# Optimization experiments

Measured on AMD Instinct MI355X. Metric: run time of the kernel, lower is better.

The kernel has to match this reference:

```python
import jax, jax.numpy as jnp
import numpy as np
from jax import lax

DIM = 96
D_STATE = 16
D_CONV = 4
EXPAND = 2
D_INNER = EXPAND * DIM           # 192
DT_RANK = (DIM + 15) // 16       # 6
EPS = 1e-5


def _upsample2x_align_corners(x):
    # bilinear, align_corners=True, scale_factor=2 (matches nn.Upsample)
    B, C, H, W = x.shape
    def lin_idx(n_in, n_out):
        pos = jnp.arange(n_out) * ((n_in - 1) / (n_out - 1))
        i0 = jnp.floor(pos).astype(jnp.int32)
        i1 = jnp.minimum(i0 + 1, n_in - 1)
        w = (pos - i0).astype(x.dtype)
        return i0, i1, w
    r0, r1, rw = lin_idx(H, 2 * H)
    c0, c1, cw = lin_idx(W, 2 * W)
    xr = x[:, :, r0, :] * (1 - rw)[None, None, :, None] + x[:, :, r1, :] * rw[None, None, :, None]
    return xr[:, :, :, c0] * (1 - cw) + xr[:, :, :, c1] * cw


def _conv2d(x, w, b, pad):
    y = lax.conv_general_dilated(x, w, (1, 1), [(pad, pad), (pad, pad)],
                                 dimension_numbers=('NCHW', 'OIHW', 'NCHW'))
    return y + b[None, :, None, None]


def _instance_norm(x):
    m = x.mean(axis=(2, 3), keepdims=True)
    v = x.var(axis=(2, 3), keepdims=True)
    return (x - m) * lax.rsqrt(v + EPS)


def _selective_scan(u, dt, A, Bm, Cm, D):
    # u, dt: [B,L,Din]; Bm, Cm: [B,L,N]; A: [Din,N]; D: [Din]
    def step(h, inp):
        u_t, dt_t, B_t, C_t = inp                       # [B,Din],[B,Din],[B,N],[B,N]
        dA = jnp.exp(dt_t[..., None] * A)               # [B,Din,N]
        h = h * dA + (dt_t * u_t)[..., None] * B_t[:, None, :]
        y = jnp.einsum('bdn,bn->bd', h, C_t)
        return h, y
    Bsz, L, Din = u.shape
    h0 = jnp.zeros((Bsz, Din, A.shape[1]), u.dtype)
    xs = (u.swapaxes(0, 1), dt.swapaxes(0, 1), Bm.swapaxes(0, 1), Cm.swapaxes(0, 1))
    _, ys = lax.scan(step, h0, xs)                      # ys: [L,B,Din]
    return ys.swapaxes(0, 1) + u * D


def _mamba(xseq, in_proj_w, conv1d_w, conv1d_b, x_proj_w, dt_proj_w, dt_proj_b,
           A_log, D, out_proj_w):
    # xseq: [B,L,dim]
    xz = xseq @ in_proj_w.T                             # [B,L,2*Din]
    xin, z = jnp.split(xz, 2, axis=-1)
    xc = xin.swapaxes(1, 2)                             # [B,Din,L]
    xc = lax.conv_general_dilated(xc, conv1d_w, (1,), [(D_CONV - 1, 0)],
                                  dimension_numbers=('NCH', 'OIH', 'NCH'),
                                  feature_group_count=D_INNER)
    xc = xc + conv1d_b[None, :, None]
    u = jax.nn.silu(xc.swapaxes(1, 2))                  # [B,L,Din]
    x_dbl = u @ x_proj_w.T                              # [B,L,dt_rank+2N]
    dt, Bm, Cm = jnp.split(x_dbl, [DT_RANK, DT_RANK + D_STATE], axis=-1)
    dt = jax.nn.softplus(dt @ dt_proj_w.T + dt_proj_b)  # [B,L,Din]
    A = -jnp.exp(A_log)                                 # [Din,N]
    y = _selective_scan(u, dt, A, Bm, Cm, D)
    y = y * jax.nn.silu(z)
    return y @ out_proj_w.T                             # [B,L,dim]


def setup_inputs() -> dict:
    key = jax.random.key(0)
    ks = jax.random.split(key, 16)
    s = 0.05
    inp = {
        'x': jax.random.normal(ks[0], (2, DIM, 64, 64), jnp.float32),
        'Hx': jax.random.normal(ks[1], (2, DIM * 2, 128, 128), jnp.float32),
        'conv1_w': jax.random.normal(ks[2], (DIM, DIM * 3, 1, 1), jnp.float32) * s,
        'conv1_b': jax.random.normal(ks[3], (DIM,), jnp.float32) * s,
        'conv2_w': jax.random.normal(ks[4], (DIM, DIM, 3, 3), jnp.float32) * s,
        'conv2_b': jax.random.normal(ks[5], (DIM,), jnp.float32) * s,
        'conv3_w': jax.random.normal(ks[6], (DIM, DIM, 1, 1), jnp.float32) * s,
        'conv3_b': jax.random.normal(ks[7], (DIM,), jnp.float32) * s,
        'in_proj_w': jax.random.normal(ks[8], (2 * D_INNER, DIM), jnp.float32) * s,
        'conv1d_w': jax.random.normal(ks[9], (D_INNER, 1, D_CONV), jnp.float32) * s,
        'conv1d_b': jax.random.normal(ks[10], (D_INNER,), jnp.float32) * s,
        'x_proj_w': jax.random.normal(ks[11], (DT_RANK + 2 * D_STATE, D_INNER), jnp.float32) * s,
        'dt_proj_w': jax.random.normal(ks[12], (D_INNER, DT_RANK), jnp.float32) * s,
        'dt_proj_b': jax.random.normal(ks[13], (D_INNER,), jnp.float32) * 0.1,
        'A_log': jnp.log(jnp.tile(jnp.arange(1, D_STATE + 1, dtype=jnp.float32)[None, :], (D_INNER, 1))),
        'D': jnp.ones((D_INNER,), jnp.float32),
        'out_proj_w': jax.random.normal(ks[14], (DIM, D_INNER), jnp.float32) * s,
    }
    return inp


def reference(x, Hx, conv1_w, conv1_b, conv2_w, conv2_b, conv3_w, conv3_b,
              in_proj_w, conv1d_w, conv1d_b, x_proj_w, dt_proj_w, dt_proj_b,
              A_log, D, out_proj_w):
    up = _upsample2x_align_corners(x)                   # [B,dim,H,W]
    cat = jnp.concatenate([up, Hx], axis=1)             # [B,3*dim,H,W]
    h = _conv2d(cat, conv1_w, conv1_b, 0)
    h = _conv2d(h, conv2_w, conv2_b, 1)
    h = _conv2d(h, conv3_w, conv3_b, 0)
    Lx = jax.nn.selu(_instance_norm(h))                 # [B,dim,H,W]
    B, C, H, W = Lx.shape
    seq = Lx.reshape(B, C, H * W).swapaxes(1, 2)        # [B,L,dim]
    y = _mamba(seq, in_proj_w, conv1d_w, conv1d_b, x_proj_w, dt_proj_w,
               dt_proj_b, A_log, D, out_proj_w)
    return y.swapaxes(1, 2).reshape(B, C, H, W) + Lx
```

## Files before the change

### kernel.cpp

```cpp
#include <hip/hip_runtime.h>
#include <hip/hip_bf16.h>
#include <math.h>

#define LSEQ 16384
#define DIN  192
#define GCH  512
#define TCH  32

typedef float f4v __attribute__((ext_vector_type(4)));
typedef short s8v __attribute__((ext_vector_type(8)));
typedef unsigned short u16x8 __attribute__((ext_vector_type(8)));

__device__ __forceinline__ float siluf(float x) { return __fdividef(x, 1.0f + __expf(-x)); }
__device__ __forceinline__ float fexp2(float x) {
#if __has_builtin(__builtin_amdgcn_exp2f)
  return __builtin_amdgcn_exp2f(x);
#else
  return __expf(x * 0.69314718056f);
#endif
}
__device__ __forceinline__ unsigned short f2bf(float f) {
  unsigned int u = __float_as_uint(f);
  unsigned int r = (u + 0x7FFFu + ((u >> 16) & 1u)) >> 16;
  return (unsigned short)r;
}
__device__ __forceinline__ float bf2f(unsigned short s) {
  return __uint_as_float(((unsigned int)s) << 16);
}

__global__ __launch_bounds__(256) void k_packw(const float* __restrict__ c1w,
    const float* __restrict__ c2w, const float* __restrict__ c3w,
    const float* __restrict__ Win, const float* __restrict__ Wx,
    const float* __restrict__ Wout, unsigned short* __restrict__ P) {
  int i = blockIdx.x * 256 + threadIdx.x;
  if (i >= 184320) return;
  if (i < 27648) { P[i] = f2bf(c1w[i]); return; }
  int j = i - 27648;
  if (j < 82944) {
    int cc = j / 27648, r = j - cc * 27648;
    int kk = r / 3072, r2 = r - kk * 3072;
    int oc = r2 >> 5, icl = r2 & 31;
    int ky = kk / 3, kx = kk - ky * 3;
    P[i] = f2bf(c2w[((oc * 96 + cc * 32 + icl) * 3 + ky) * 3 + kx]);
    return;
  }
  j -= 82944;
  if (j < 9216) { P[i] = f2bf(c3w[j]); return; }
  j -= 9216;
  if (j < 36864) { P[i] = f2bf(Win[j]); return; }
  j -= 36864;
  if (j < 9216) {
    int oc = j / 192, k = j - oc * 192;
    P[i] = (oc < 38) ? f2bf(Wx[oc * 192 + k]) : (unsigned short)0;
    return;
  }
  j -= 9216;
  P[i] = f2bf(Wout[j]);
}

__global__ __launch_bounds__(256) void k_upcat(const float* __restrict__ x,
    const float* __restrict__ Hx, unsigned short* __restrict__ UH) {
  __shared__ float tile[96 * 65];
  int px0 = blockIdx.x * 64, b = blockIdx.y;
  int tid = threadIdx.x;
  for (int cg = 0; cg < 3; cg++) {
    if (cg == 0) {
      int oh = px0 >> 7, owbase = px0 & 127;
      float pr = oh * (63.0f / 127.0f);
      int r0 = (int)pr; float rw = pr - (float)r0; int r1 = min(r0 + 1, 63);
      for (int t = tid; t < 1536; t += 256) {
        int c = t >> 4, p4 = t & 15;
        const float* rp0 = x + ((size_t)b * 96 + c) * 4096 + r0 * 64;
        const float* rp1 = x + ((size_t)b * 96 + c) * 4096 + r1 * 64;
#pragma unroll
        for (int g = 0; g < 4; g++) {
          int ow = owbase + p4 * 4 + g;
          float pc = ow * (63.0f / 127.0f);
          int c0 = (int)pc; float cw = pc - (float)c0; int c1 = min(c0 + 1, 63);
          float v00 = rp0[c0], v01 = rp0[c1], v10 = rp1[c0], v11 = rp1[c1];
          float top = v00 + (v10 - v00) * rw;
          float bot = v01 + (v11 - v01) * rw;
          tile[c * 65 + p4 * 4 + g] = top + (bot - top) * cw;
        }
      }
    } else {
      for (int t = tid; t < 1536; t += 256) {
        int c = t >> 4, p4 = t & 15;
        float4 v = *(const float4*)&Hx[((size_t)b * 192 + (cg - 1) * 96 + c) * LSEQ + px0 + p4 * 4];
        tile[c * 65 + p4 * 4 + 0] = v.x;
        tile[c * 65 + p4 * 4 + 1] = v.y;
        tile[c * 65 + p4 * 4 + 2] = v.z;
        tile[c * 65 + p4 * 4 + 3] = v.w;
      }
    }
    __syncthreads();
    for (int t = tid; t < 768; t += 256) {
      int px = t / 12, c8 = t - px * 12;
      u16x8 o;
#pragma unroll
      for (int jj = 0; jj < 8; jj++) o[jj] = f2bf(tile[(c8 * 8 + jj) * 65 + px]);
      *(u16x8*)&UH[((size_t)b * LSEQ + px0 + px) * 288 + cg * 96 + c8 * 8] = o;
    }
    __syncthreads();
  }
}

#define OUT_BF16R    0
#define OUT_F32P     1
#define OUT_F32R     2
#define OUT_F32P_RES 4
#define OUT_XZ       5

template<int OM, int NT>
__global__ __launch_bounds__(256) void k_gemm(
    const unsigned short* __restrict__ X,
    const unsigned short* __restrict__ Wp, const float* __restrict__ bias,
    void* __restrict__ outv, void* __restrict__ outv2, const float* __restrict__ resid,
    int K, int ostride, int ng) {
  __shared__ unsigned short x_t[128 * 96];
  __shared__ unsigned short w_t[NT * 16 * 96];
  Wp += (size_t)blockIdx.y * 96 * K;
  int pxg0 = blockIdx.x * 128;
  int b = pxg0 >> 14, px_in0 = pxg0 & 16383;
  int tid = threadIdx.x, lane = tid & 63, wv = tid >> 6;
  int r = lane & 15, q = lane >> 4;
  f4v acc[2][NT];
#pragma unroll
  for (int mi = 0; mi < 2; mi++)
#pragma unroll
    for (int n = 0; n < NT; n++) acc[mi][n] = (f4v)0.0f;
  int nchunk = K / 96;
  for (int kc = 0; kc < nchunk; kc++) {
    for (int t = tid; t < NT * 16 * 12; t += 256) {
      int row = t / 12, u8 = t - row * 12;
      *(u16x8*)&w_t[row * 96 + u8 * 8] = *(const u16x8*)&Wp[(size_t)row * K + kc * 96 + u8 * 8];
    }
    for (int t = tid; t < 1536; t += 256) {
      int rr = t / 12, u8 = t - rr * 12;
      *(u16x8*)&x_t[rr * 96 + u8 * 8] =
          *(const u16x8*)&X[(size_t)(pxg0 + rr) * K + kc * 96 + u8 * 8];
    }
    __syncthreads();
#pragma unroll
    for (int k0 = 0; k0 < 96; k0 += 32) {
      s8v a0 = *(const s8v*)&x_t[((wv * 2 + 0) * 16 + r) * 96 + k0 + q * 8];
      s8v a1 = *(const s8v*)&x_t[((wv * 2 + 1) * 16 + r) * 96 + k0 + q * 8];
#pragma unroll
      for (int n = 0; n < NT; n++) {
        s8v bb = *(const s8v*)&w_t[(n * 16 + r) * 96 + k0 + q * 8];
        acc[0][n] = __builtin_amdgcn_mfma_f32_16x16x32_bf16(a0, bb, acc[0][n], 0, 0, 0);
        acc[1][n] = __builtin_amdgcn_mfma_f32_16x16x32_bf16(a1, bb, acc[1][n], 0, 0, 0);
      }
    }
    __syncthreads();
  }
#pragma unroll
  for (int mi = 0; mi < 2; mi++) {
    int pxl = (wv * 2 + mi) * 16 + q * 4;
    int pxg = pxg0 + pxl;
#pragma unroll
    for (int n = 0; n < NT; n++) {
      int oc = n * 16 + r;
      if (OM == OUT_BF16R) {
        float bv = bias[oc];
        unsigned short* O = (unsigned short*)outv;
#pragma unroll
        for (int g = 0; g < 4; g++)
          O[(size_t)(pxg + g) * 96 + oc] = f2bf(acc[mi][n][g] + bv);
      } else if (OM == OUT_F32P) {
        float bv = bias[oc];
        float* O = (float*)outv;
        float4 o = make_float4(acc[mi][n][0] + bv, acc[mi][n][1] + bv,
                               acc[mi][n][2] + bv, acc[mi][n][3] + bv);
        *(float4*)&O[((size_t)b * 96 + oc) * LSEQ + px_in0 + pxl] = o;
      } else if (OM == OUT_F32P_RES) {
        float* O = (float*)outv;
        size_t ad = ((size_t)b * 96 + oc) * LSEQ + px_in0 + pxl;
        float4 rv = *(const float4*)&resid[ad];
        float4 o = make_float4(acc[mi][n][0] + rv.x, acc[mi][n][1] + rv.y,
                               acc[mi][n][2] + rv.z, acc[mi][n][3] + rv.w);
        *(float4*)&O[ad] = o;
      } else if (OM == OUT_F32R) {
        float* O = (float*)outv;
        int ocg = blockIdx.y * 96 + oc;
        if (ocg < ng) {
#pragma unroll
          for (int g = 0; g < 4; g++)
            O[(size_t)(pxg + g) * ostride + ocg] = acc[mi][n][g];
        }
      } else {
        int ocg = (blockIdx.y & 1) * 96 + oc;
        if (blockIdx.y < 2) {
          float* O = (float*)outv;
#pragma unroll
          for (int g = 0; g < 4; g++)
            O[(size_t)(pxg + g) * 192 + ocg] = acc[mi][n][g];
        } else {
          unsigned short* O = (unsigned short*)outv2;
#pragma unroll
          for (int g = 0; g < 4; g++)
            O[(size_t)(pxg + g) * 192 + ocg] = f2bf(acc[mi][n][g]);
        }
      }
    }
  }
}

__global__ __launch_bounds__(256) void k_conv3x3m(const unsigned short* __restrict__ X,
    const unsigned short* __restrict__ Wp2, const float* __restrict__ bias,
    unsigned short* __restrict__ out) {
  __shared__ unsigned short in_t[3 * 68 * 32];
  __shared__ unsigned short w_t[9 * 96 * 32];
  int bi = blockIdx.x;
  int hx = bi & 1, y = (bi >> 1) & 127, b = bi >> 8;
  int px0 = hx * 64;
  int tid = threadIdx.x, lane = tid & 63, wv = tid >> 6;
  int r = lane & 15, q = lane >> 4;
  f4v acc[6];
#pragma unroll
  for (int n = 0; n < 6; n++) acc[n] = (f4v)0.0f;
  for (int cc = 0; cc < 3; cc++) {
    for (int t = tid; t < 3456; t += 256)
      *(u16x8*)&w_t[t * 8] = *(const u16x8*)&Wp2[cc * 27648 + t * 8];
    for (int t = tid; t < 792; t += 256) {
      int row = t / 264, rem = t - row * 264;
      int c_l = rem >> 2, icq = rem & 3;
      int gy = y - 1 + row, gx = px0 - 1 + c_l;
      u16x8 v = {0, 0, 0, 0, 0, 0, 0, 0};
      if (gy >= 0 && gy < 128 && gx >= 0 && gx < 128)
        v = *(const u16x8*)&X[(((size_t)b * 128 + gy) * 128 + gx) * 96 + cc * 32 + icq * 8];
      *(u16x8*)&in_t[(row * 68 + c_l) * 32 + icq * 8] = v;
    }
    __syncthreads();
#pragma unroll
    for (int kk = 0; kk < 9; kk++) {
      int ky = kk / 3, kx = kk - ky * 3;
      s8v a = *(const s8v*)&in_t[(ky * 68 + wv * 16 + r + kx) * 32 + q * 8];
#pragma unroll
      for (int n = 0; n < 6; n++) {
        s8v bb = *(const s8v*)&w_t[(kk * 96 + n * 16 + r) * 32 + q * 8];
        acc[n] = __builtin_amdgcn_mfma_f32_16x16x32_bf16(a, bb, acc[n], 0, 0, 0);
      }
    }
    __syncthreads();
  }
  size_t rowbase = ((size_t)b * 128 + y) * 128 + px0 + wv * 16 + q * 4;
#pragma unroll
  for (int n = 0; n < 6; n++) {
    int oc = n * 16 + r;
    float bv = bias[oc];
#pragma unroll
    for (int g = 0; g < 4; g++)
      out[(rowbase + g) * 96 + oc] = f2bf(acc[n][g] + bv);
  }
}

__global__ __launch_bounds__(256) void k_stats(const float* __restrict__ h, float* __restrict__ stats) {
  int bc = blockIdx.x;
  const float* p = h + (size_t)bc * LSEQ;
  float s = 0.f, ss = 0.f;
  for (int i = threadIdx.x; i < LSEQ; i += 256) { float v = p[i]; s += v; ss = fmaf(v, v, ss); }
  __shared__ float rs[256], rss[256];
  int tid = threadIdx.x;
  rs[tid] = s; rss[tid] = ss; __syncthreads();
  for (int o = 128; o > 0; o >>= 1) {
    if (tid < o) { rs[tid] += rs[tid + o]; rss[tid] += rss[tid + o]; }
    __syncthreads();
  }
  if (tid == 0) {
    float m = rs[0] * (1.0f / LSEQ);
    float var = rss[0] * (1.0f / LSEQ) - m * m;
    stats[bc * 2] = m;
    stats[bc * 2 + 1] = rsqrtf(fmaxf(var, 0.f) + 1e-5f);
  }
}

__device__ __forceinline__ float seluf(float v) {
  const float kS = 1.0507009873554805f, kSA = 1.0507009873554805f * 1.6732632423543772f;
  return v > 0.f ? kS * v : kSA * (__expf(v) - 1.f);
}
__global__ __launch_bounds__(256) void k_normselu2(const float* __restrict__ h,
    const float* __restrict__ stats, float* __restrict__ Lx, unsigned short* __restrict__ LxR) {
  __shared__ float tile[96 * 65];
  int px0 = blockIdx.x * 64, b = blockIdx.y;
  int tid = threadIdx.x;
  for (int t = tid; t < 1536; t += 256) {
    int c = t >> 4, p4 = t & 15;
    size_t ga = ((size_t)b * 96 + c) * LSEQ + px0 + p4 * 4;
    float4 v = *(const float4*)&h[ga];
    float m = stats[(b * 96 + c) * 2], rv = stats[(b * 96 + c) * 2 + 1];
    v.x = seluf((v.x - m) * rv);
    v.y = seluf((v.y - m) * rv);
    v.z = seluf((v.z - m) * rv);
    v.w = seluf((v.w - m) * rv);
    *(float4*)&Lx[ga] = v;
    tile[c * 65 + p4 * 4 + 0] = v.x;
    tile[c * 65 + p4 * 4 + 1] = v.y;
    tile[c * 65 + p4 * 4 + 2] = v.z;
    tile[c * 65 + p4 * 4 + 3] = v.w;
  }
  __syncthreads();
  for (int t = tid; t < 768; t += 256) {
    int px = t / 12, c8 = t - px * 12;
    u16x8 o;
#pragma unroll
    for (int jj = 0; jj < 8; jj++) o[jj] = f2bf(tile[(c8 * 8 + jj) * 65 + px]);
    *(u16x8*)&LxR[((size_t)b * LSEQ + px0 + px) * 96 + c8 * 8] = o;
  }
}

__global__ __launch_bounds__(256) void k_conv1d(const float* __restrict__ xzx,
    const float* __restrict__ w1d, const float* __restrict__ b1d,
    unsigned short* __restrict__ uR) {
  int gid = blockIdx.x * 256 + threadIdx.x;
  if (gid >= 2 * LSEQ * DIN) return;
  int d = gid % DIN, bl = gid / DIN;
  int l = bl & (LSEQ - 1);
  float4 w = *(const float4*)&w1d[d * 4];
  float wv[4] = {w.x, w.y, w.z, w.w};
  float acc = b1d[d];
#pragma unroll
  for (int k = 0; k < 4; k++) {
    int lk = l - 3 + k;
    if (lk >= 0) acc = fmaf(wv[k], xzx[(size_t)(bl - 3 + k) * DIN + d], acc);
  }
  uR[gid] = f2bf(siluf(acc));
}

__global__ __launch_bounds__(192, 3) void k_scanA(const unsigned short* __restrict__ uR,
    const float* __restrict__ xdbl, const float* __restrict__ Wdt,
    const float* __restrict__ bdt, const float* __restrict__ Alog,
    float* __restrict__ chA, float* __restrict__ chB) {
  int b = blockIdx.y, g = blockIdx.x, d = threadIdx.x;
  __shared__ float Bs[TCH * 16], Dts[TCH * 8];
  for (int i = d; i < TCH * 16; i += 192) {
    int t = i >> 4, n = i & 15;
    Bs[i] = xdbl[(size_t)(b * LSEQ + g * TCH + t) * 38 + 6 + n];
  }
  for (int i = d; i < TCH * 6; i += 192) {
    int t = i / 6, c = i - t * 6;
    Dts[t * 8 + c] = xdbl[(size_t)(b * LSEQ + g * TCH + t) * 38 + c];
  }
  float ac2[16];
#pragma unroll
  for (int n = 0; n < 16; n++) ac2[n] = -__expf(Alog[d * 16 + n]) * 1.44269504f;
  float wdt[6];
#pragma unroll
  for (int c = 0; c < 6; c++) wdt[c] = Wdt[d * 6 + c];
  float bd = bdt[d];
  size_t base0 = (size_t)(b * LSEQ + g * TCH);
  float uu[TCH];
#pragma unroll
  for (int t = 0; t < TCH; t++) uu[t] = bf2f(uR[(base0 + t) * DIN + d]);
  __syncthreads();
  float dtv[TCH];
#pragma unroll
  for (int t = 0; t < TCH; t++) {
    float dr = bd;
#pragma unroll
    for (int c = 0; c < 6; c++) dr = fmaf(Dts[t * 8 + c], wdt[c], dr);
    dtv[t] = dr > 20.f ? dr : __logf(1.f + __expf(dr));
  }
  float ap[16], hb[16];
#pragma unroll
  for (int n = 0; n < 16; n++) { ap[n] = 1.f; hb[n] = 0.f; }
#pragma unroll
  for (int t = 0; t < TCH; t++) {
    float du = dtv[t] * uu[t];
    float bs[16];
    const float4* src = (const float4*)&Bs[t * 16];
#pragma unroll
    for (int qq = 0; qq < 4; qq++) {
      float4 v = src[qq];
      bs[qq * 4] = v.x; bs[qq * 4 + 1] = v.y; bs[qq * 4 + 2] = v.z; bs[qq * 4 + 3] = v.w;
    }
#pragma unroll
    for (int n = 0; n < 16; n++) {
      float e = fexp2(dtv[t] * ac2[n]);
      ap[n] *= e;
      hb[n] = fmaf(hb[n], e, du * bs[n]);
    }
  }
  size_t co = ((size_t)(b * GCH + g) * DIN + d) * 16;
#pragma unroll
  for (int qq = 0; qq < 4; qq++) {
    ((float4*)(chA + co))[qq] = make_float4(ap[qq * 4], ap[qq * 4 + 1], ap[qq * 4 + 2], ap[qq * 4 + 3]);
    ((float4*)(chB + co))[qq] = make_float4(hb[qq * 4], hb[qq * 4 + 1], hb[qq * 4 + 2], hb[qq * 4 + 3]);
  }
}

__global__ __launch_bounds__(256) void k_scanB(const float* __restrict__ chA,
    const float* __restrict__ chB, float* __restrict__ h0) {
  __shared__ float sa[16 * 17], sb[16 * 17];
  int blk = blockIdx.x;
  int b = blk / DIN, d = blk - b * DIN;
  int tid = threadIdx.x;
  int seg = tid >> 4, n = tid & 15;
  float ca[32], cb[32];
  float aagg = 1.f, bagg = 0.f;
#pragma unroll 8
  for (int j = 0; j < 32; j++) {
    int g = seg * 32 + j;
    size_t off = ((size_t)(b * GCH + g) * DIN + d) * 16 + n;
    float a = chA[off], bb = chB[off];
    ca[j] = a; cb[j] = bb;
    bagg = fmaf(a, bagg, bb);
    aagg *= a;
  }
  sa[n * 17 + seg] = aagg;
  sb[n * 17 + seg] = bagg;
  __syncthreads();
  if (tid < 16) {
    float pa = 1.f, pb = 0.f;
#pragma unroll
    for (int s = 0; s < 16; s++) {
      float ta = sa[tid * 17 + s], tb = sb[tid * 17 + s];
      sa[tid * 17 + s] = pa;
      sb[tid * 17 + s] = pb;
      pb = fmaf(ta, pb, tb);
      pa *= ta;
    }
  }
  __syncthreads();
  float h = sb[n * 17 + seg];
#pragma unroll 8
  for (int j = 0; j < 32; j++) {
    int g = seg * 32 + j;
    size_t off = ((size_t)(b * GCH + g) * DIN + d) * 16 + n;
    h0[off] = h;
    h = fmaf(ca[j], h, cb[j]);
  }
}

__global__ __launch_bounds__(192, 3) void k_scanC(const unsigned short* __restrict__ uR,
    const float* __restrict__ xdbl, const float* __restrict__ Wdt,
    const float* __restrict__ bdt, const unsigned short* __restrict__ zR,
    const float* __restrict__ Alog, const float* __restrict__ Dp,
    const float* __restrict__ h0, unsigned short* __restrict__ yR) {
  int b = blockIdx.y, g = blockIdx.x, d = threadIdx.x;
  __shared__ float Bs[TCH * 16], Cs[TCH * 16], Dts[TCH * 8];
  for (int i = d; i < TCH * 16; i += 192) {
    int t = i >> 4, n = i & 15;
    size_t rb = (size_t)(b * LSEQ + g * TCH + t) * 38;
    Bs[i] = xdbl[rb + 6 + n];
    Cs[i] = xdbl[rb + 22 + n];
  }
  for (int i = d; i < TCH * 6; i += 192) {
    int t = i / 6, c = i - t * 6;
    Dts[t * 8 + c] = xdbl[(size_t)(b * LSEQ + g * TCH + t) * 38 + c];
  }
  float ac2[16];
#pragma unroll
  for (int n = 0; n < 16; n++) ac2[n] = -__expf(Alog[d * 16 + n]) * 1.44269504f;
  float wdt[6];
#pragma unroll
  for (int c = 0; c < 6; c++) wdt[c] = Wdt[d * 6 + c];
  float bd = bdt[d];
  float Dd = Dp[d];
  size_t base0 = (size_t)(b * LSEQ + g * TCH);
  float uu[TCH];
#pragma unroll
  for (int t = 0; t < TCH; t++) uu[t] = bf2f(uR[(base0 + t) * DIN + d]);
  size_t co = ((size_t)(b * GCH + g) * DIN + d) * 16;
  float h[16];
#pragma unroll
  for (int qq = 0; qq < 4; qq++) {
    float4 v = ((const float4*)(h0 + co))[qq];
    h[qq * 4] = v.x; h[qq * 4 + 1] = v.y; h[qq * 4 + 2] = v.z; h[qq * 4 + 3] = v.w;
  }
  __syncthreads();
  float dtv[TCH];
#pragma unroll
  for (int t = 0; t < TCH; t++) {
    float dr = bd;
#pragma unroll
    for (int c = 0; c < 6; c++) dr = fmaf(Dts[t * 8 + c], wdt[c], dr);
    dtv[t] = dr > 20.f ? dr : __logf(1.f + __expf(dr));
  }
#pragma unroll
  for (int t = 0; t < TCH; t++) {
    float du = dtv[t] * uu[t];
    float zv = bf2f(zR[(base0 + t) * DIN + d]);
    float bs[16], cs[16];
    const float4* sbp = (const float4*)&Bs[t * 16];
    const float4* scp = (const float4*)&Cs[t * 16];
#pragma unroll
    for (int qq = 0; qq < 4; qq++) {
      float4 vb = sbp[qq], vc = scp[qq];
      bs[qq * 4] = vb.x; bs[qq * 4 + 1] = vb.y; bs[qq * 4 + 2] = vb.z; bs[qq * 4 + 3] = vb.w;
      cs[qq * 4] = vc.x; cs[qq * 4 + 1] = vc.y; cs[qq * 4 + 2] = vc.z; cs[qq * 4 + 3] = vc.w;
    }
    float y0 = 0.f, y1 = 0.f, y2 = 0.f, y3 = 0.f;
#pragma unroll
    for (int n = 0; n < 16; n++) {
      float e = fexp2(dtv[t] * ac2[n]);
      h[n] = fmaf(h[n], e, du * bs[n]);
      float p = h[n] * cs[n];
      if ((n & 3) == 0) y0 += p; else if ((n & 3) == 1) y1 += p;
      else if ((n & 3) == 2) y2 += p; else y3 += p;
    }
    float yv = ((y0 + y1) + (y2 + y3)) + uu[t] * Dd;
    yR[(base0 + t) * DIN + d] = f2bf(yv * siluf(zv));
  }
}

extern "C" void kernel_launch(void* const* d_in, const int* in_sizes, int n_in,
                              void* d_out, int out_size, void* d_ws, size_t ws_size,
                              hipStream_t stream) {
  (void)in_sizes; (void)n_in; (void)out_size; (void)ws_size;
  const float* x    = (const float*)d_in[0];
  const float* Hx   = (const float*)d_in[1];
  const float* c1w  = (const float*)d_in[2];
  const float* c1b  = (const float*)d_in[3];
  const float* c2w  = (const float*)d_in[4];
  const float* c2b  = (const float*)d_in[5];
  const float* c3w  = (const float*)d_in[6];
  const float* c3b  = (const float*)d_in[7];
  const float* Win  = (const float*)d_in[8];
  const float* w1d  = (const float*)d_in[9];
  const float* b1d  = (const float*)d_in[10];
  const float* Wx   = (const float*)d_in[11];
  const float* Wdt  = (const float*)d_in[12];
  const float* bdt  = (const float*)d_in[13];
  const float* Alog = (const float*)d_in[14];
  const float* Dp   = (const float*)d_in[15];
  const float* Wout = (const float*)d_in[16];
  float* out = (float*)d_out;

  float* ws = (float*)d_ws;
  const size_t F = (size_t)2 * 96 * LSEQ;
  const size_t Fh = F / 2;

  float*          b_h3 = ws;
  float*          chA  = ws;
  float*          b_Lx = ws + F;
  unsigned short* R1   = (unsigned short*)(ws + 2 * F);
  unsigned short* R2   = (unsigned short*)(ws + 2 * F + Fh);
  float*          xdbl = ws + 2 * F + Fh;
  unsigned short* UH   = (unsigned short*)(ws + 3 * F);
  float*          xzx  = ws + 3 * F;
  float*          chB  = ws + 3 * F;
  unsigned short* yRb  = (unsigned short*)(ws + 3 * F);
  float*          h0b  = ws + 4 * F;
  unsigned short* zRb  = (unsigned short*)(ws + 5 * F);
  unsigned short* R3   = (unsigned short*)(ws + 6 * F);
  unsigned short* Wp   = (unsigned short*)(ws + 7 * F);
  float*          b_st = ws + 7 * F + 92160;

  k_packw<<<dim3(720), dim3(256), 0, stream>>>(c1w, c2w, c3w, Win, Wx, Wout, Wp);
  k_upcat<<<dim3(256, 2), dim3(256), 0, stream>>>(x, Hx, UH);
  k_gemm<OUT_BF16R, 6><<<dim3(256, 1), dim3(256), 0, stream>>>(
      UH, Wp, c1b, R1, nullptr, nullptr, 288, 0, 0);
  k_conv3x3m<<<dim3(512), dim3(256), 0, stream>>>(R1, Wp + 27648, c2b, R2);
  k_gemm<OUT_F32P, 6><<<dim3(256, 1), dim3(256), 0, stream>>>(
      R2, Wp + 110592, c3b, b_h3, nullptr, nullptr, 96, 0, 0);
  k_stats<<<dim3(192), dim3(256), 0, stream>>>(b_h3, b_st);
  k_normselu2<<<dim3(256, 2), dim3(256), 0, stream>>>(b_h3, b_st, b_Lx, R1);
  k_gemm<OUT_XZ, 6><<<dim3(256, 4), dim3(256), 0, stream>>>(
      R1, Wp + 119808, nullptr, xzx, zRb, nullptr, 96, 192, 0);
  k_conv1d<<<dim3((2 * LSEQ * DIN + 255) / 256), dim3(256), 0, stream>>>(xzx, w1d, b1d, R3);
  k_gemm<OUT_F32R, 3><<<dim3(256, 1), dim3(256), 0, stream>>>(
      R3, Wp + 156672, nullptr, xdbl, nullptr, nullptr, 192, 38, 38);
  k_scanA<<<dim3(GCH, 2), dim3(192), 0, stream>>>(R3, xdbl, Wdt, bdt, Alog, chA, chB);
  k_scanB<<<dim3(2 * DIN), dim3(256), 0, stream>>>(chA, chB, h0b);
  k_scanC<<<dim3(GCH, 2), dim3(192), 0, stream>>>(R3, xdbl, Wdt, bdt, zRb, Alog, Dp, h0b, yRb);
  k_gemm<OUT_F32P_RES, 6><<<dim3(256, 1), dim3(256), 0, stream>>>(
      yRb, Wp + 165888, nullptr, out, nullptr, b_Lx, 192, 0, 0);
}
```

Before: 333.9 us.

## Fuse instance-norm stats into conv3 GEMM and store xz projection as bf16

The conv3 GEMM epilogue now accumulates per-channel sum and sum-of-squares through shared-memory and global atomics, which removes the separate stats kernel. The stats buffer is zeroed inside the weight-pack kernel, and the norm kernel derives mean and rstd from the raw sums. The in_proj GEMM now uses 12 N-tiles over 2 y-blocks and writes the x branch as bf16 instead of fp32, which halves that traffic into conv1d. The scan also preloads the z values up front, and the workspace layout is reshuffled. The one-pass E[x²]−m² variance computed with float atomics may lose precision and is not deterministic.

```diff
diff --git a/kernel.cpp b/kernel.cpp
--- a/kernel.cpp
+++ b/kernel.cpp
@@ -31,9 +31,10 @@
 __global__ __launch_bounds__(256) void k_packw(const float* __restrict__ c1w,
     const float* __restrict__ c2w, const float* __restrict__ c3w,
     const float* __restrict__ Win, const float* __restrict__ Wx,
-    const float* __restrict__ Wout, unsigned short* __restrict__ P) {
+    const float* __restrict__ Wout, unsigned short* __restrict__ P,
+    float* __restrict__ st) {
   int i = blockIdx.x * 256 + threadIdx.x;
-  if (i >= 184320) return;
+  if (i >= 184320) { if (i < 184704) st[i - 184320] = 0.f; return; }
   if (i < 27648) { P[i] = f2bf(c1w[i]); return; }
   int j = i - 27648;
   if (j < 82944) {
@@ -105,11 +106,11 @@
   }
 }
 
-#define OUT_BF16R    0
-#define OUT_F32P     1
-#define OUT_F32R     2
-#define OUT_F32P_RES 4
-#define OUT_XZ       5
+#define OUT_BF16R       0
+#define OUT_F32R        2
+#define OUT_F32P_RES    4
+#define OUT_F32P_STATS  6
+#define OUT_XZB         7
 
 template<int OM, int NT>
 __global__ __launch_bounds__(256) void k_gemm(
@@ -119,7 +120,8 @@
     int K, int ostride, int ng) {
   __shared__ unsigned short x_t[128 * 96];
   __shared__ unsigned short w_t[NT * 16 * 96];
-  Wp += (size_t)blockIdx.y * 96 * K;
+  __shared__ float sstat[(OM == OUT_F32P_STATS) ? 192 : 2];
+  Wp += (size_t)blockIdx.y * NT * 16 * K;
   int pxg0 = blockIdx.x * 128;
   int b = pxg0 >> 14, px_in0 = pxg0 & 16383;
   int tid = threadIdx.x, lane = tid & 63, wv = tid >> 6;
@@ -154,6 +156,10 @@
     }
     __syncthreads();
   }
+  if (OM == OUT_F32P_STATS) {
+    if (tid < 192) sstat[tid] = 0.f;
+    __syncthreads();
+  }
 #pragma unroll
   for (int mi = 0; mi < 2; mi++) {
     int pxl = (wv * 2 + mi) * 16 + q * 4;
@@ -167,12 +173,16 @@
 #pragma unroll
         for (int g = 0; g < 4; g++)
           O[(size_t)(pxg + g) * 96 + oc] = f2bf(acc[mi][n][g] + bv);
-      } else if (OM == OUT_F32P) {
+      } else if (OM == OUT_F32P_STATS) {
         float bv = bias[oc];
         float* O = (float*)outv;
         float4 o = make_float4(acc[mi][n][0] + bv, acc[mi][n][1] + bv,
                                acc[mi][n][2] + bv, acc[mi][n][3] + bv);
         *(float4*)&O[((size_t)b * 96 + oc) * LSEQ + px_in0 + pxl] = o;
+        float s = o.x + o.y + o.z + o.w;
+        float qsum = o.x * o.x + o.y * o.y + o.z * o.z + o.w * o.w;
+        atomicAdd(&sstat[oc * 2], s);
+        atomicAdd(&sstat[oc * 2 + 1], qsum);
       } else if (OM == OUT_F32P_RES) {
         float* O = (float*)outv;
         size_t ad = ((size_t)b * 96 + oc) * LSEQ + px_in0 + pxl;
@@ -182,26 +192,26 @@
         *(float4*)&O[ad] = o;
       } else if (OM == OUT_F32R) {
         float* O = (float*)outv;
-        int ocg = blockIdx.y * 96 + oc;
+        int ocg = blockIdx.y * NT * 16 + oc;
         if (ocg < ng) {
 #pragma unroll
           for (int g = 0; g < 4; g++)
             O[(size_t)(pxg + g) * ostride + ocg] = acc[mi][n][g];
         }
       } else {
-        int ocg = (blockIdx.y & 1) * 96 + oc;
-        if (blockIdx.y < 2) {
-          float* O = (float*)outv;
-#pragma unroll
-          for (int g = 0; g < 4; g++)
-            O[(size_t)(pxg + g) * 192 + ocg] = acc[mi][n][g];
-        } else {
-          unsigned short* O = (unsigned short*)outv2;
-#pragma unroll
-          for (int g = 0; g < 4; g++)
-            O[(size_t)(pxg + g) * 192 + ocg] = f2bf(acc[mi][n][g]);
-        }
+        unsigned short* O = (blockIdx.y == 0) ? (unsigned short*)outv : (unsigned short*)outv2;
+#pragma unroll
+        for (int g = 0; g < 4; g++)
+          O[(size_t)(pxg + g) * 192 + oc] = f2bf(acc[mi][n][g]);
       }
+    }
+  }
+  if (OM == OUT_F32P_STATS) {
+    __syncthreads();
+    if (tid < 96) {
+      float* statsg = (float*)outv2;
+      atomicAdd(&statsg[(b * 96 + tid) * 2], sstat[tid * 2]);
+      atomicAdd(&statsg[(b * 96 + tid) * 2 + 1], sstat[tid * 2 + 1]);
     }
   }
 }
@@ -255,26 +265,6 @@
   }
 }
 
-__global__ __launch_bounds__(256) void k_stats(const float* __restrict__ h, float* __restrict__ stats) {
-  int bc = blockIdx.x;
-  const float* p = h + (size_t)bc * LSEQ;
-  float s = 0.f, ss = 0.f;
-  for (int i = threadIdx.x; i < LSEQ; i += 256) { float v = p[i]; s += v; ss = fmaf(v, v, ss); }
-  __shared__ float rs[256], rss[256];
-  int tid = threadIdx.x;
-  rs[tid] = s; rss[tid] = ss; __syncthreads();
-  for (int o = 128; o > 0; o >>= 1) {
-    if (tid < o) { rs[tid] += rs[tid + o]; rss[tid] += rss[tid + o]; }
-    __syncthreads();
-  }
-  if (tid == 0) {
-    float m = rs[0] * (1.0f / LSEQ);
-    float var = rss[0] * (1.0f / LSEQ) - m * m;
-    stats[bc * 2] = m;
-    stats[bc * 2 + 1] = rsqrtf(fmaxf(var, 0.f) + 1e-5f);
-  }
-}
-
 __device__ __forceinline__ float seluf(float v) {
   const float kS = 1.0507009873554805f, kSA = 1.0507009873554805f * 1.6732632423543772f;
   return v > 0.f ? kS * v : kSA * (__expf(v) - 1.f);
@@ -288,7 +278,10 @@
     int c = t >> 4, p4 = t & 15;
     size_t ga = ((size_t)b * 96 + c) * LSEQ + px0 + p4 * 4;
     float4 v = *(const float4*)&h[ga];
-    float m = stats[(b * 96 + c) * 2], rv = stats[(b * 96 + c) * 2 + 1];
+    float S1 = stats[(b * 96 + c) * 2], S2 = stats[(b * 96 + c) * 2 + 1];
+    float m = S1 * (1.0f / LSEQ);
+    float var = S2 * (1.0f / LSEQ) - m * m;
+    float rv = rsqrtf(fmaxf(var, 0.f) + 1e-5f);
     v.x = seluf((v.x - m) * rv);
     v.y = seluf((v.y - m) * rv);
     v.z = seluf((v.z - m) * rv);
@@ -309,7 +302,7 @@
   }
 }
 
-__global__ __launch_bounds__(256) void k_conv1d(const float* __restrict__ xzx,
+__global__ __launch_bounds__(256) void k_conv1d(const unsigned short* __restrict__ xzx,
     const float* __restrict__ w1d, const float* __restrict__ b1d,
     unsigned short* __restrict__ uR) {
   int gid = blockIdx.x * 256 + threadIdx.x;
@@ -322,7 +315,7 @@
 #pragma unroll
   for (int k = 0; k < 4; k++) {
     int lk = l - 3 + k;
-    if (lk >= 0) acc = fmaf(wv[k], xzx[(size_t)(bl - 3 + k) * DIN + d], acc);
+    if (lk >= 0) acc = fmaf(wv[k], bf2f(xzx[(size_t)(bl - 3 + k) * DIN + d]), acc);
   }
   uR[gid] = f2bf(siluf(acc));
 }
@@ -458,9 +451,11 @@
   float bd = bdt[d];
   float Dd = Dp[d];
   size_t base0 = (size_t)(b * LSEQ + g * TCH);
-  float uu[TCH];
+  float uu[TCH], zz[TCH];
 #pragma unroll
   for (int t = 0; t < TCH; t++) uu[t] = bf2f(uR[(base0 + t) * DIN + d]);
+#pragma unroll
+  for (int t = 0; t < TCH; t++) zz[t] = bf2f(zR[(base0 + t) * DIN + d]);
   size_t co = ((size_t)(b * GCH + g) * DIN + d) * 16;
   float h[16];
 #pragma unroll
@@ -480,7 +475,6 @@
 #pragma unroll
   for (int t = 0; t < TCH; t++) {
     float du = dtv[t] * uu[t];
-    float zv = bf2f(zR[(base0 + t) * DIN + d]);
     float bs[16], cs[16];
     const float4* sbp = (const float4*)&Bs[t * 16];
     const float4* scp = (const float4*)&Cs[t * 16];
@@ -500,7 +494,7 @@
       else if ((n & 3) == 2) y2 += p; else y3 += p;
     }
     float yv = ((y0 + y1) + (y2 + y3)) + uu[t] * Dd;
-    yR[(base0 + t) * DIN + d] = f2bf(yv * siluf(zv));
+    yR[(base0 + t) * DIN + d] = f2bf(yv * siluf(zz[t]));
   }
 }
 
@@ -531,34 +525,33 @@
   const size_t F = (size_t)2 * 96 * LSEQ;
   const size_t Fh = F / 2;
 
-  float*          b_h3 = ws;
+  unsigned short* UH   = (unsigned short*)ws;
   float*          chA  = ws;
-  float*          b_Lx = ws + F;
-  unsigned short* R1   = (unsigned short*)(ws + 2 * F);
-  unsigned short* R2   = (unsigned short*)(ws + 2 * F + Fh);
-  float*          xdbl = ws + 2 * F + Fh;
-  unsigned short* UH   = (unsigned short*)(ws + 3 * F);
-  float*          xzx  = ws + 3 * F;
-  float*          chB  = ws + 3 * F;
-  unsigned short* yRb  = (unsigned short*)(ws + 3 * F);
-  float*          h0b  = ws + 4 * F;
-  unsigned short* zRb  = (unsigned short*)(ws + 5 * F);
-  unsigned short* R3   = (unsigned short*)(ws + 6 * F);
-  unsigned short* Wp   = (unsigned short*)(ws + 7 * F);
-  float*          b_st = ws + 7 * F + 92160;
-
-  k_packw<<<dim3(720), dim3(256), 0, stream>>>(c1w, c2w, c3w, Win, Wx, Wout, Wp);
+  unsigned short* R1   = (unsigned short*)(ws + F + Fh);
+  float*          b_h3 = ws + 2 * F;
+  float*          h0b  = ws + 2 * F;
+  float*          b_Lx = ws + 3 * F;
+  unsigned short* R2   = (unsigned short*)(ws + 4 * F);
+  float*          xdbl = ws + 4 * F;
+  unsigned short* xzxR = (unsigned short*)(ws + 5 * F);
+  float*          chB  = ws + 5 * F;
+  unsigned short* yRb  = (unsigned short*)(ws + 5 * F);
+  unsigned short* zRb  = (unsigned short*)(ws + 6 * F);
+  unsigned short* R3   = (unsigned short*)(ws + 7 * F);
+  unsigned short* Wp   = (unsigned short*)(ws + 8 * F);
+  float*          b_st = ws + 8 * F + 92160;
+
+  k_packw<<<dim3(722), dim3(256), 0, stream>>>(c1w, c2w, c3w, Win, Wx, Wout, Wp, b_st);
   k_upcat<<<dim3(256, 2), dim3(256), 0, stream>>>(x, Hx, UH);
   k_gemm<OUT_BF16R, 6><<<dim3(256, 1), dim3(256), 0, stream>>>(
       UH, Wp, c1b, R1, nullptr, nullptr, 288, 0, 0);
   k_conv3x3m<<<dim3(512), dim3(256), 0, stream>>>(R1, Wp + 27648, c2b, R2);
-  k_gemm<OUT_F32P, 6><<<dim3(256, 1), dim3(256), 0, stream>>>(
-      R2, Wp + 110592, c3b, b_h3, nullptr, nullptr, 96, 0, 0);
-  k_stats<<<dim3(192), dim3(256), 0, stream>>>(b_h3, b_st);
+  k_gemm<OUT_F32P_STATS, 6><<<dim3(256, 1), dim3(256), 0, stream>>>(
+      R2, Wp + 110592, c3b, b_h3, b_st, nullptr, 96, 0, 0);
   k_normselu2<<<dim3(256, 2), dim3(256), 0, stream>>>(b_h3, b_st, b_Lx, R1);
-  k_gemm<OUT_XZ, 6><<<dim3(256, 4), dim3(256), 0, stream>>>(
-      R1, Wp + 119808, nullptr, xzx, zRb, nullptr, 96, 192, 0);
-  k_conv1d<<<dim3((2 * LSEQ * DIN + 255) / 256), dim3(256), 0, stream>>>(xzx, w1d, b1d, R3);
+  k_gemm<OUT_XZB, 12><<<dim3(256, 2), dim3(256), 0, stream>>>(
+      R1, Wp + 119808, nullptr, xzxR, zRb, nullptr, 96, 192, 0);
+  k_conv1d<<<dim3((2 * LSEQ * DIN + 255) / 256), dim3(256), 0, stream>>>(xzxR, w1d, b1d, R3);
   k_gemm<OUT_F32R, 3><<<dim3(256, 1), dim3(256), 0, stream>>>(
       R3, Wp + 156672, nullptr, xdbl, nullptr, nullptr, 192, 38, 38);
   k_scanA<<<dim3(GCH, 2), dim3(192), 0, stream>>>(R3, xdbl, Wdt, bdt, Alog, chA, chB);
```

New measurement: 438.6 us. 1.31x slower.
